# Kernel optimization log

Measured on AMD Instinct MI355X. Metric: run time of the kernel, lower is better.

## Reference

```python
import jax, jax.numpy as jnp
import numpy as np

N_USERS = 50000
N0, N1, N2 = 200000, 50000, 12500
E0, E1, E2 = 1600000, 400000, 100000
B = 128
NUMP, TWEET, CATP, DES = 6, 768, 2, 768
IN_DIM, HID = 128, 128
SLOPE = 0.01  # LeakyReLU default


def setup_inputs() -> dict:
    key = jax.random.key(0)
    ks = iter(jax.random.split(key, 32))
    f32 = jnp.float32
    nrm = lambda s, sc=0.05: jax.random.normal(next(ks), s, f32) * sc
    inp = {}
    inp['x_raw'] = jax.random.normal(next(ks), (N_USERS, NUMP + TWEET + CATP + DES), f32)
    inp['W_des'] = nrm((DES, IN_DIM // 4)); inp['b_des'] = jnp.zeros((IN_DIM // 4,), f32)
    inp['W_tweet'] = nrm((TWEET, IN_DIM // 4)); inp['b_tweet'] = jnp.zeros((IN_DIM // 4,), f32)
    inp['W_num'] = nrm((NUMP, IN_DIM // 4)); inp['b_num'] = jnp.zeros((IN_DIM // 4,), f32)
    inp['W_cat'] = nrm((CATP, IN_DIM // 4)); inp['b_cat'] = jnp.zeros((IN_DIM // 4,), f32)
    inp['W_in'] = nrm((IN_DIM, HID)); inp['b_in'] = jnp.zeros((HID,), f32)
    inp['prelu_a'] = jnp.full((HID,), 0.25, f32)
    inp['W_conv'] = nrm((3, HID, HID)); inp['b_conv'] = jnp.zeros((3, HID), f32)
    inp['Wc1'] = nrm((3 * HID, HID)); inp['bc1'] = jnp.zeros((HID,), f32)
    inp['Wc2'] = nrm((HID, HID)); inp['bc2'] = jnp.zeros((HID,), f32)
    ri = lambda n, hi: jax.random.randint(next(ks), (n,), 0, hi, jnp.int32)
    inp['nodelist'] = ri(N0, N_USERS)
    inp['e0'] = jnp.stack([ri(E0, N0), ri(E0, N0)])
    inp['e1'] = jnp.stack([ri(E1, N1), ri(E1, N1)])
    inp['e2'] = jnp.stack([ri(E2, N2), ri(E2, N2)])
    inp['parent1'] = ri(N0, N1)   # coarsening assignment layer0 -> layer1
    inp['parent2'] = ri(N1, N2)   # layer1 -> layer2
    inp['batch1'] = jnp.sort(ri(N1, B))
    inp['batch2'] = jnp.sort(ri(N2, B))
    return inp


def _leaky(x):
    return jnp.where(x > 0, x, SLOPE * x)


def _gcn(h, ei, W, b, n):
    # GCNConv: lin -> sym-normalized add-aggregation with self-loops -> +bias
    h = h @ W
    loop = jnp.arange(n, dtype=ei.dtype)
    src = jnp.concatenate([ei[0], loop])
    dst = jnp.concatenate([ei[1], loop])
    deg = jax.ops.segment_sum(jnp.ones(dst.shape, h.dtype), dst, num_segments=n)
    dinv = jnp.where(deg > 0, jax.lax.rsqrt(deg), 0.0)
    msg = h[src] * (dinv[src] * dinv[dst])[:, None]
    return jax.ops.segment_sum(msg, dst, num_segments=n) + b


def reference(x_raw, W_des, b_des, W_tweet, b_tweet, W_num, b_num, W_cat, b_cat,
              W_in, b_in, prelu_a, W_conv, b_conv, Wc1, bc1, Wc2, bc2,
              nodelist, e0, e1, e2, parent1, parent2, batch1, batch2):
    # FeatureEncoder (twibot-20 slicing order: num_prop | tweet | cat_prop | des)
    n = _leaky(x_raw[:, :NUMP] @ W_num + b_num)
    t = _leaky(x_raw[:, NUMP:NUMP + TWEET] @ W_tweet + b_tweet)
    c = _leaky(x_raw[:, NUMP + TWEET:NUMP + TWEET + CATP] @ W_cat + b_cat)
    d = _leaky(x_raw[:, NUMP + TWEET + CATP:] @ W_des + b_des)
    h = jnp.concatenate([d, t, n, c], axis=1) @ W_in + b_in
    enc = jnp.where(h > 0, h, prelu_a * h)  # PReLU

    x = enc[nodelist]  # [N0, HID] gather per batched nodelists
    edges = [e0, e1, e2]
    sizes = [N0, N1, N2]
    parents = [parent1, parent2]
    nxt = [N1, N2]
    xs = []
    for i in range(3):
        x = jax.nn.relu(_gcn(x, edges[i], W_conv[i], b_conv[i], sizes[i]))
        if i < 2:  # SEPooling: pure scatter-add onto parent nodes (nn unused in its forward)
            x = jax.nn.relu(jax.ops.segment_sum(x, parents[i], num_segments=nxt[i]))
        xs.append(x)
    pooled = jnp.concatenate([
        jax.ops.segment_sum(xs[0], batch1, num_segments=B),
        jax.ops.segment_sum(xs[1], batch2, num_segments=B),
        jax.ops.segment_sum(xs[2], batch2, num_segments=B),
    ], axis=1)  # global sum pool, batch at layer min(i+1, tree_depth-1)
    z = jax.nn.relu(pooled @ Wc1 + bc1)  # dropout inactive (eval)
    return z @ Wc2 + bc2
```

## Files before the change

kernel.cpp:

```cpp
#include <hip/hip_runtime.h>

#define N_USERS 50000
#define NN0 200000
#define NN1 50000
#define NN2 12500
#define EE0 1600000
#define EE1 400000
#define EE2 100000


__global__ __launch_bounds__(256) void k_enc3(
    const float* __restrict__ xr,
    const float* __restrict__ Wd, const float* __restrict__ bd,
    const float* __restrict__ Wt, const float* __restrict__ bt,
    const float* __restrict__ Wn, const float* __restrict__ bn,
    const float* __restrict__ Wc, const float* __restrict__ bc,
    float* __restrict__ h128)
{
    __shared__ float XsD[32][68];
    __shared__ float XsT[32][68];
    __shared__ float Ws[32][68];
    __shared__ float xnc[64][8];
    __shared__ float Wl[8][64];

    int t = threadIdx.x;
    int cg = t & 15, rg = t >> 4;
    int base = blockIdx.x * 64;

    if (t < 64) {
        int row = base + t;
        if (row < N_USERS) {
            const float* xp = xr + (size_t)row * 1544;
            float4 a = *(const float4*)xp;
            float2 b2 = *(const float2*)(xp + 4);
            float2 c2 = *(const float2*)(xp + 774);
            xnc[t][0] = a.x; xnc[t][1] = a.y; xnc[t][2] = a.z; xnc[t][3] = a.w;
            xnc[t][4] = b2.x; xnc[t][5] = b2.y; xnc[t][6] = c2.x; xnc[t][7] = c2.y;
        } else {
            #pragma unroll
            for (int k = 0; k < 8; k++) xnc[t][k] = 0.f;
        }
    } else if (t >= 192) {
        int l = t - 192;
        #pragma unroll
        for (int k = 0; k < 8; k++) {
            float w = 0.f;
            if (l < 32) { if (k < 6) w = Wn[k * 32 + l]; }
            else        { if (k >= 6) w = Wc[(k - 6) * 32 + (l - 32)]; }
            Wl[k][l] = w;
        }
    }

    float acc[4][4];
    #pragma unroll
    for (int r = 0; r < 4; r++)
        #pragma unroll
        for (int c = 0; c < 4; c++) acc[r][c] = 0.f;

    for (int kc = 0; kc < 768; kc += 32) {
        __syncthreads();
        #pragma unroll
        for (int h = 0; h < 2; h++) {
            int fi = t * 2 + h;
            int row = fi >> 3, q = fi & 7;
            int grow = base + row;
            float4 vd = {0.f, 0.f, 0.f, 0.f};
            float2 va = {0.f, 0.f}, vb = {0.f, 0.f};
            if (grow < N_USERS) {
                const float* xp = xr + (size_t)grow * 1544 + kc + q * 4;
                vd = *(const float4*)(xp + 776);
                va = *(const float2*)(xp + 6);
                vb = *(const float2*)(xp + 8);
            }
            int k0 = q * 4;
            XsD[k0 + 0][row] = vd.x; XsD[k0 + 1][row] = vd.y;
            XsD[k0 + 2][row] = vd.z; XsD[k0 + 3][row] = vd.w;
            XsT[k0 + 0][row] = va.x; XsT[k0 + 1][row] = va.y;
            XsT[k0 + 2][row] = vb.x; XsT[k0 + 3][row] = vb.y;
        }
        #pragma unroll
        for (int h = 0; h < 2; h++) {
            int fi = t + h * 256;
            int k = fi >> 4, c4 = (fi & 15) * 4;
            float4 w = (c4 < 32) ? *(const float4*)(Wd + (size_t)(kc + k) * 32 + c4)
                                 : *(const float4*)(Wt + (size_t)(kc + k) * 32 + (c4 - 32));
            *(float4*)&Ws[k][c4] = w;
        }
        __syncthreads();

        const float* Xp = (cg < 8) ? &XsD[0][0] : &XsT[0][0];
        #pragma unroll 8
        for (int k = 0; k < 32; k++) {
            float4 xv = *(const float4*)(Xp + k * 68 + rg * 4);
            float4 wv = *(const float4*)&Ws[k][cg * 4];
            acc[0][0] = fmaf(xv.x, wv.x, acc[0][0]);
            acc[0][1] = fmaf(xv.x, wv.y, acc[0][1]);
            acc[0][2] = fmaf(xv.x, wv.z, acc[0][2]);
            acc[0][3] = fmaf(xv.x, wv.w, acc[0][3]);
            acc[1][0] = fmaf(xv.y, wv.x, acc[1][0]);
            acc[1][1] = fmaf(xv.y, wv.y, acc[1][1]);
            acc[1][2] = fmaf(xv.y, wv.z, acc[1][2]);
            acc[1][3] = fmaf(xv.y, wv.w, acc[1][3]);
            acc[2][0] = fmaf(xv.z, wv.x, acc[2][0]);
            acc[2][1] = fmaf(xv.z, wv.y, acc[2][1]);
            acc[2][2] = fmaf(xv.z, wv.z, acc[2][2]);
            acc[2][3] = fmaf(xv.z, wv.w, acc[2][3]);
            acc[3][0] = fmaf(xv.w, wv.x, acc[3][0]);
            acc[3][1] = fmaf(xv.w, wv.y, acc[3][1]);
            acc[3][2] = fmaf(xv.w, wv.z, acc[3][2]);
            acc[3][3] = fmaf(xv.w, wv.w, acc[3][3]);
        }
    }

    float bh[4], bl[4], wlv[8][4];
    #pragma unroll
    for (int c = 0; c < 4; c++) {
        int j = cg * 4 + c;
        bh[c] = (j < 32) ? bd[j] : bt[j - 32];
        bl[c] = (j < 32) ? bn[j] : bc[j - 32];
        #pragma unroll
        for (int k = 0; k < 8; k++) wlv[k][c] = Wl[k][j];
    }
    #pragma unroll
    for (int r = 0; r < 4; r++) {
        int lr = rg * 4 + r;
        int row = base + lr;
        if (row >= N_USERS) break;
        float4 hv;
        float* ph = &hv.x;
        #pragma unroll
        for (int c = 0; c < 4; c++) {
            float v = acc[r][c] + bh[c];
            ph[c] = v > 0.f ? v : 0.01f * v;
        }
        *(float4*)(h128 + (size_t)row * 128 + cg * 4) = hv;
        float4 lv;
        float* pl = &lv.x;
        #pragma unroll
        for (int c = 0; c < 4; c++) {
            float v = bl[c];
            #pragma unroll
            for (int k = 0; k < 8; k++) v = fmaf(xnc[lr][k], wlv[k][c], v);
            pl[c] = v > 0.f ? v : 0.01f * v;
        }
        *(float4*)(h128 + (size_t)row * 128 + 64 + cg * 4) = lv;
    }
}

template<int EPI>
__global__ __launch_bounds__(256) void k_gemmT(
    const float* X, const float* __restrict__ W, const float* __restrict__ bias,
    const float* __restrict__ pa, float* OUT, int n)
{
    __shared__ float Xs[32][132];
    __shared__ float Ws[32][132];
    int t = threadIdx.x;
    int cg = t & 31, rg = t >> 5;
    int base = blockIdx.x * 32;

    #pragma unroll
    for (int h = 0; h < 4; h++) {
        int fi = t + h * 256;
        int row = fi >> 5, q = fi & 31;
        float4 v = {0.f, 0.f, 0.f, 0.f};
        if (base + row < n) v = *(const float4*)(X + (size_t)(base + row) * 128 + q * 4);
        *(float4*)&Xs[row][q * 4] = v;
    }

    float acc[4][4];
    #pragma unroll
    for (int r = 0; r < 4; r++)
        #pragma unroll
        for (int c = 0; c < 4; c++) acc[r][c] = 0.f;

    for (int kc = 0; kc < 128; kc += 32) {
        __syncthreads();
        #pragma unroll
        for (int h = 0; h < 4; h++) {
            int fi = t + h * 256;
            int k = fi >> 5, q = fi & 31;
            *(float4*)&Ws[k][q * 4] = *(const float4*)(W + (size_t)(kc + k) * 128 + q * 4);
        }
        __syncthreads();
        #pragma unroll
        for (int k4 = 0; k4 < 8; k4++) {
            int k = k4 * 4;
            float4 w0 = *(const float4*)&Ws[k + 0][cg * 4];
            float4 w1 = *(const float4*)&Ws[k + 1][cg * 4];
            float4 w2 = *(const float4*)&Ws[k + 2][cg * 4];
            float4 w3 = *(const float4*)&Ws[k + 3][cg * 4];
            #pragma unroll
            for (int r = 0; r < 4; r++) {
                float4 xv = *(const float4*)&Xs[rg * 4 + r][kc + k];
                acc[r][0] = fmaf(xv.w, w3.x, fmaf(xv.z, w2.x, fmaf(xv.y, w1.x, fmaf(xv.x, w0.x, acc[r][0]))));
                acc[r][1] = fmaf(xv.w, w3.y, fmaf(xv.z, w2.y, fmaf(xv.y, w1.y, fmaf(xv.x, w0.y, acc[r][1]))));
                acc[r][2] = fmaf(xv.w, w3.z, fmaf(xv.z, w2.z, fmaf(xv.y, w1.z, fmaf(xv.x, w0.z, acc[r][2]))));
                acc[r][3] = fmaf(xv.w, w3.w, fmaf(xv.z, w2.w, fmaf(xv.y, w1.w, fmaf(xv.x, w0.w, acc[r][3]))));
            }
        }
    }

    float4 bv = {0.f, 0.f, 0.f, 0.f}, pv = {0.f, 0.f, 0.f, 0.f};
    if (EPI == 1) { bv = *(const float4*)(bias + cg * 4); pv = *(const float4*)(pa + cg * 4); }
    #pragma unroll
    for (int r = 0; r < 4; r++) {
        int row = base + rg * 4 + r;
        if (row >= n) break;
        float4 v;
        if (EPI == 1) {
            v.x = acc[r][0] + bv.x; v.x = v.x > 0.f ? v.x : pv.x * v.x;
            v.y = acc[r][1] + bv.y; v.y = v.y > 0.f ? v.y : pv.y * v.y;
            v.z = acc[r][2] + bv.z; v.z = v.z > 0.f ? v.z : pv.z * v.z;
            v.w = acc[r][3] + bv.w; v.w = v.w > 0.f ? v.w : pv.w * v.w;
        } else {
            v.x = acc[r][0]; v.y = acc[r][1]; v.z = acc[r][2]; v.w = acc[r][3];
        }
        *(float4*)(OUT + (size_t)row * 128 + cg * 4) = v;
    }
}

__device__ __forceinline__ void seg_of_scanblk(int b, int& doff, int& bsoff, int& lb) {
    if (b < 196)      { doff = 0;      bsoff = 0;   lb = b; }
    else if (b < 245) { doff = 200704; bsoff = 196; lb = b - 196; }
    else if (b < 258) { doff = 250880; bsoff = 245; lb = b - 245; }
    else if (b < 307) { doff = 264192; bsoff = 258; lb = b - 258; }
    else              { doff = 314368; bsoff = 307; lb = b - 307; }
}

__global__ __launch_bounds__(256) void k_count_all(
    const int* __restrict__ d0, const int* __restrict__ d1, const int* __restrict__ d2,
    const int* __restrict__ p1, const int* __restrict__ p2,
    int* __restrict__ degs, int* __restrict__ ranks)
{
    int t0 = blockIdx.x * 256 + threadIdx.x;
    if (t0 >= 587500) return;
    #pragma unroll
    for (int k = 0; k < 4; k++) {
        int gid = t0 + k * 587500;
        int idx;
        if (gid < 1600000)      idx = d0[gid];
        else if (gid < 2000000) idx = 200704 + d1[gid - 1600000];
        else if (gid < 2100000) idx = 250880 + d2[gid - 2000000];
        else if (gid < 2300000) idx = 264192 + p1[gid - 2100000];
        else                    idx = 314368 + p2[gid - 2300000];
        ranks[gid] = atomicAdd(&degs[idx], 1);
    }
}

__global__ __launch_bounds__(256) void k_scan_all(
    const int* __restrict__ degs, int* __restrict__ rowsts, int* __restrict__ bsums)
{
    __shared__ int sh[256];
    int doff, bsoff, lb;
    seg_of_scanblk(blockIdx.x, doff, bsoff, lb);
    int t = threadIdx.x;
    int base = doff + lb * 1024 + t * 4;
    int v[4], s = 0;
    #pragma unroll
    for (int k = 0; k < 4; k++) { v[k] = degs[base + k]; s += v[k]; }
    sh[t] = s;
    __syncthreads();
    for (int off = 1; off < 256; off <<= 1) {
        int x = 0;
        if (t >= off) x = sh[t - off];
        __syncthreads();
        if (t >= off) sh[t] += x;
        __syncthreads();
    }
    int ex = sh[t] - s;
    if (t == 255) bsums[bsoff + lb] = sh[255];
    #pragma unroll
    for (int k = 0; k < 4; k++) { rowsts[base + k] = ex; ex += v[k]; }
}

__global__ __launch_bounds__(256) void k_scantop_all(int* __restrict__ bsums)
{
    __shared__ int sh[256];
    int b = blockIdx.x;
    int off0, nb;
    if (b == 0)      { off0 = 0;   nb = 196; }
    else if (b == 1) { off0 = 196; nb = 49; }
    else if (b == 2) { off0 = 245; nb = 13; }
    else if (b == 3) { off0 = 258; nb = 49; }
    else             { off0 = 307; nb = 13; }
    int t = threadIdx.x;
    int v = (t < nb) ? bsums[off0 + t] : 0;
    sh[t] = v;
    __syncthreads();
    for (int off = 1; off < 256; off <<= 1) {
        int x = 0;
        if (t >= off) x = sh[t - off];
        __syncthreads();
        if (t >= off) sh[t] += x;
        __syncthreads();
    }
    if (t < nb) bsums[off0 + t] = sh[t] - v;
}

__global__ __launch_bounds__(256) void k_scanadd_all(
    int* __restrict__ rowsts, const int* __restrict__ bsums,
    const int* __restrict__ degs, float* __restrict__ dinvs)
{
    int doff, bsoff, lb;
    seg_of_scanblk(blockIdx.x, doff, bsoff, lb);
    int t = threadIdx.x;
    int base = doff + lb * 1024 + t * 4;
    int add = bsums[bsoff + lb];
    bool dodinv = (doff <= 250880);
    #pragma unroll
    for (int k = 0; k < 4; k++) {
        int i = base + k;
        rowsts[i] += add;
        if (dodinv) dinvs[i] = rsqrtf((float)degs[i] + 1.0f);
    }
}

__global__ __launch_bounds__(256) void k_scatter_all(
    const int* __restrict__ s0, const int* __restrict__ d0,
    const int* __restrict__ s1, const int* __restrict__ d1,
    const int* __restrict__ s2, const int* __restrict__ d2,
    const int* __restrict__ p1, const int* __restrict__ p2,
    const int* __restrict__ rowsts, const int* __restrict__ ranks,
    int* __restrict__ elists)
{
    int t0 = blockIdx.x * 256 + threadIdx.x;
    if (t0 >= 587500) return;
    #pragma unroll
    for (int k = 0; k < 4; k++) {
        int gid = t0 + k * 587500;
        int idx, val, eloff;
        if (gid < 1600000)      { idx = d0[gid];                    val = s0[gid];           eloff = 0; }
        else if (gid < 2000000) { int i = gid - 1600000; idx = 200704 + d1[i]; val = s1[i]; eloff = 1600000; }
        else if (gid < 2100000) { int i = gid - 2000000; idx = 250880 + d2[i]; val = s2[i]; eloff = 2000000; }
        else if (gid < 2300000) { int i = gid - 2100000; idx = 264192 + p1[i]; val = i;     eloff = 2100000; }
        else                    { int i = gid - 2300000; idx = 314368 + p2[i]; val = i;     eloff = 2300000; }
        int p = rowsts[idx] + ranks[gid];
        elists[eloff + p] = val;
    }
}

__global__ __launch_bounds__(256) void k_gatherU(
    const float* __restrict__ U, const int* __restrict__ nl,
    const int* __restrict__ rowst, const int* __restrict__ elist,
    const float* __restrict__ dinv, const float* __restrict__ bias,
    float* __restrict__ out, int n)
{
    size_t gid = (size_t)blockIdx.x * 256 + threadIdx.x;
    int d = (int)(gid >> 5);
    if (d >= n) return;
    int l = (int)(gid & 31);
    const float4* Uv = (const float4*)U;
    float dd = dinv[d];
    float4 self = Uv[(size_t)nl[d] * 32 + l];
    float4 acc;
    acc.x = self.x * dd; acc.y = self.y * dd; acc.z = self.z * dd; acc.w = self.w * dd;
    int s0 = rowst[d], s1 = rowst[d + 1];
    for (int e = s0; e < s1; ++e) {
        int s = elist[e];
        float ds = dinv[s];
        float4 v = Uv[(size_t)nl[s] * 32 + l];
        acc.x = fmaf(v.x, ds, acc.x);
        acc.y = fmaf(v.y, ds, acc.y);
        acc.z = fmaf(v.z, ds, acc.z);
        acc.w = fmaf(v.w, ds, acc.w);
    }
    const float4 b = ((const float4*)bias)[l];
    float4 y;
    y.x = fmaxf(fmaf(acc.x, dd, b.x), 0.f);
    y.y = fmaxf(fmaf(acc.y, dd, b.y), 0.f);
    y.z = fmaxf(fmaf(acc.z, dd, b.z), 0.f);
    y.w = fmaxf(fmaf(acc.w, dd, b.w), 0.f);
    ((float4*)out)[(size_t)d * 32 + l] = y;
}

__global__ __launch_bounds__(256) void k_gather(
    const float* __restrict__ h, const int* __restrict__ rowst,
    const int* __restrict__ elist, const float* __restrict__ dinv,
    const float* __restrict__ bias, float* __restrict__ out, int n)
{
    size_t gid = (size_t)blockIdx.x * 256 + threadIdx.x;
    int d = (int)(gid >> 5);
    if (d >= n) return;
    int l = (int)(gid & 31);
    const float4* hv = (const float4*)h;
    float dd = dinv[d];
    float4 self = hv[(size_t)d * 32 + l];
    float4 acc;
    acc.x = self.x * dd; acc.y = self.y * dd; acc.z = self.z * dd; acc.w = self.w * dd;
    int s0 = rowst[d], s1 = rowst[d + 1];
    for (int e = s0; e < s1; ++e) {
        int s = elist[e];
        float ds = dinv[s];
        float4 v = hv[(size_t)s * 32 + l];
        acc.x = fmaf(v.x, ds, acc.x);
        acc.y = fmaf(v.y, ds, acc.y);
        acc.z = fmaf(v.z, ds, acc.z);
        acc.w = fmaf(v.w, ds, acc.w);
    }
    const float4 b = ((const float4*)bias)[l];
    float4 y;
    y.x = fmaxf(fmaf(acc.x, dd, b.x), 0.f);
    y.y = fmaxf(fmaf(acc.y, dd, b.y), 0.f);
    y.z = fmaxf(fmaf(acc.z, dd, b.z), 0.f);
    y.w = fmaxf(fmaf(acc.w, dd, b.w), 0.f);
    ((float4*)out)[(size_t)d * 32 + l] = y;
}

__global__ __launch_bounds__(256) void k_poolgather(
    const float* __restrict__ Y, const int* __restrict__ rowst,
    const int* __restrict__ elist, float* __restrict__ out, int np)
{
    size_t gid = (size_t)blockIdx.x * 256 + threadIdx.x;
    int p = (int)(gid >> 5);
    if (p >= np) return;
    int l = (int)(gid & 31);
    const float4* yv = (const float4*)Y;
    float4 acc = {0.f, 0.f, 0.f, 0.f};
    int s0 = rowst[p], s1 = rowst[p + 1];
    for (int e = s0; e < s1; ++e) {
        int i = elist[e];
        float4 v = yv[(size_t)i * 32 + l];
        acc.x += v.x; acc.y += v.y; acc.z += v.z; acc.w += v.w;
    }
    float4 y;
    y.x = fmaxf(acc.x, 0.f); y.y = fmaxf(acc.y, 0.f);
    y.z = fmaxf(acc.z, 0.f); y.w = fmaxf(acc.w, 0.f);
    ((float4*)out)[(size_t)p * 32 + l] = y;
}

__global__ __launch_bounds__(128) void k_bpool_all(
    const float* __restrict__ X1, const float* __restrict__ X2, const float* __restrict__ Y2,
    const int* __restrict__ b1, const int* __restrict__ b2, float* __restrict__ pl)
{
    int b = blockIdx.x;
    const float* src; const int* bidx; int coloff, n, r0;
    if (b < 391)      { src = X1; bidx = b1; coloff = 0;   n = 50000; r0 = b * 128; }
    else if (b < 489) { src = X2; bidx = b2; coloff = 128; n = 12500; r0 = (b - 391) * 128; }
    else              { src = Y2; bidx = b2; coloff = 256; n = 12500; r0 = (b - 489) * 128; }
    if (r0 >= n) return;
    int j = threadIdx.x;
    int r1 = min(r0 + 128, n);
    float acc = 0.f;
    int prev = bidx[r0];
    for (int r = r0; r < r1; ++r) {
        int bb = bidx[r];
        if (bb != prev) {
            unsafeAtomicAdd(&pl[(size_t)prev * 384 + coloff + j], acc);
            acc = 0.f; prev = bb;
        }
        acc += src[(size_t)r * 128 + j];
    }
    unsafeAtomicAdd(&pl[(size_t)prev * 384 + coloff + j], acc);
}

__global__ void k_mlp(const float* __restrict__ A, const float* __restrict__ W,
                      const float* __restrict__ b, float* __restrict__ out,
                      int K, int dorelu)
{
    __shared__ float as[384];
    int r = blockIdx.x, j = threadIdx.x;
    for (int i = j; i < K; i += 128) as[i] = A[(size_t)r * K + i];
    __syncthreads();
    float acc = b[j];
    for (int k = 0; k < K; k++) acc = fmaf(as[k], W[(size_t)k * 128 + j], acc);
    if (dorelu) acc = fmaxf(acc, 0.f);
    out[(size_t)r * 128 + j] = acc;
}

extern "C" void kernel_launch(void* const* d_in, const int* in_sizes, int n_in,
                              void* d_out, int out_size, void* d_ws, size_t ws_size,
                              hipStream_t stream)
{
    const float* x_raw  = (const float*)d_in[0];
    const float* W_des  = (const float*)d_in[1];
    const float* b_des  = (const float*)d_in[2];
    const float* W_twe  = (const float*)d_in[3];
    const float* b_twe  = (const float*)d_in[4];
    const float* W_num  = (const float*)d_in[5];
    const float* b_num  = (const float*)d_in[6];
    const float* W_cat  = (const float*)d_in[7];
    const float* b_cat  = (const float*)d_in[8];
    const float* W_in   = (const float*)d_in[9];
    const float* b_in   = (const float*)d_in[10];
    const float* prelua = (const float*)d_in[11];
    const float* W_conv = (const float*)d_in[12];
    const float* b_conv = (const float*)d_in[13];
    const float* Wc1    = (const float*)d_in[14];
    const float* bc1    = (const float*)d_in[15];
    const float* Wc2    = (const float*)d_in[16];
    const float* bc2    = (const float*)d_in[17];
    const int* nodelist = (const int*)d_in[18];
    const int* e0       = (const int*)d_in[19];
    const int* e1       = (const int*)d_in[20];
    const int* e2       = (const int*)d_in[21];
    const int* parent1  = (const int*)d_in[22];
    const int* parent2  = (const int*)d_in[23];
    const int* batch1   = (const int*)d_in[24];
    const int* batch2   = (const int*)d_in[25];

    float* WS  = (float*)d_ws;
    float* ENC = WS;
    int*   DEGS   = (int*)d_ws;
    int*   ROWSTS = DEGS + 327680;
    float* DINVS  = (float*)(ROWSTS + 327680);
    int*   BSUMS  = (int*)(DINVS + 264192);
    int*   RANKS  = BSUMS + 512;
    int*   ELISTS = RANKS + 2350000;
    float* U  = WS + 6400000;
    float* H  = WS + 12800000;
    float* Y  = WS + 19200000;
    float* X1 = WS + 44800000;
    float* X2 = WS + 51200000;
    float* PL = WS + 52800000;
    float* Z  = PL + 49152;

    hipMemsetAsync(PL, 0, (size_t)128 * 384 * 4, stream);

    k_enc3<<<(N_USERS + 63) / 64, 256, 0, stream>>>(
        x_raw, W_des, b_des, W_twe, b_twe, W_num, b_num, W_cat, b_cat, ENC);
    k_gemmT<1><<<(N_USERS + 31) / 32, 256, 0, stream>>>(
        ENC, W_in, b_in, prelua, ENC, N_USERS);
    k_gemmT<0><<<(N_USERS + 31) / 32, 256, 0, stream>>>(
        ENC, W_conv, nullptr, nullptr, U, N_USERS);

    hipMemsetAsync(DEGS, 0, (size_t)327680 * 4, stream);
    k_count_all<<<(587500 + 255) / 256, 256, 0, stream>>>(
        e0 + EE0, e1 + EE1, e2 + EE2, parent1, parent2, DEGS, RANKS);
    k_scan_all<<<320, 256, 0, stream>>>(DEGS, ROWSTS, BSUMS);
    k_scantop_all<<<5, 256, 0, stream>>>(BSUMS);
    k_scanadd_all<<<320, 256, 0, stream>>>(ROWSTS, BSUMS, DEGS, DINVS);
    k_scatter_all<<<(587500 + 255) / 256, 256, 0, stream>>>(
        e0, e0 + EE0, e1, e1 + EE1, e2, e2 + EE2, parent1, parent2,
        ROWSTS, RANKS, ELISTS);

    k_gatherU<<<(int)(((size_t)NN0 * 32 + 255) / 256), 256, 0, stream>>>(
        U, nodelist, ROWSTS, ELISTS, DINVS, b_conv, Y, NN0);
    k_poolgather<<<(int)(((size_t)NN1 * 32 + 255) / 256), 256, 0, stream>>>(
        Y, ROWSTS + 264192, ELISTS + 2100000, X1, NN1);

    k_gemmT<0><<<(NN1 + 31) / 32, 256, 0, stream>>>(
        X1, W_conv + 16384, nullptr, nullptr, H, NN1);
    k_gather<<<(int)(((size_t)NN1 * 32 + 255) / 256), 256, 0, stream>>>(
        H, ROWSTS + 200704, ELISTS + 1600000, DINVS + 200704, b_conv + 128, Y, NN1);
    k_poolgather<<<(int)(((size_t)NN2 * 32 + 255) / 256), 256, 0, stream>>>(
        Y, ROWSTS + 314368, ELISTS + 2300000, X2, NN2);

    k_gemmT<0><<<(NN2 + 31) / 32, 256, 0, stream>>>(
        X2, W_conv + 32768, nullptr, nullptr, H, NN2);
    k_gather<<<(int)(((size_t)NN2 * 32 + 255) / 256), 256, 0, stream>>>(
        H, ROWSTS + 250880, ELISTS + 2000000, DINVS + 250880, b_conv + 256, Y, NN2);

    k_bpool_all<<<587, 128, 0, stream>>>(X1, X2, Y, batch1, batch2, PL);

    k_mlp<<<128, 128, 0, stream>>>(PL, Wc1, bc1, Z, 384, 1);
    k_mlp<<<128, 128, 0, stream>>>(Z, Wc2, bc2, (float*)d_out, 128, 0);
}
```

Measured before the change: 753.5 us.

## Fuse GCN aggregation with pooling, chain encoder GEMMs, prefetch encoder tiles, merge MLP

Several fusions land together. The encoder's input-projection GEMM and the first conv-weight GEMM now run in one kernel that keeps the PReLU output in shared memory. Each GCN gather is fused with the following parent pooling, so per-node outputs Y are no longer written and re-read. The separate scan-top kernel is replaced by a per-block reduction inside scanadd, the two MLP launches are merged, and the k_enc3 loads are register-prefetched one K-chunk ahead. Together these cut launches and intermediate global traffic. The cost is more register pressure and work grouped by parent node, which may leave the load imbalanced across threads.

Result: slower. 848.6 us (+12.6%).

```diff
diff --git a/kernel.cpp b/kernel.cpp
--- a/kernel.cpp
+++ b/kernel.cpp
@@ -51,6 +51,31 @@
         }
     }
 
+    int srow[2], sq[2];
+    #pragma unroll
+    for (int h = 0; h < 2; h++) { int fi = t * 2 + h; srow[h] = fi >> 3; sq[h] = fi & 7; }
+    bool vr[2];
+    #pragma unroll
+    for (int h = 0; h < 2; h++) vr[h] = (base + srow[h]) < N_USERS;
+
+    float4 pvd[2]; float2 pva[2], pvb[2]; float4 pw[2];
+
+    #pragma unroll
+    for (int h = 0; h < 2; h++) {
+        pvd[h] = make_float4(0.f, 0.f, 0.f, 0.f);
+        pva[h] = make_float2(0.f, 0.f); pvb[h] = make_float2(0.f, 0.f);
+        if (vr[h]) {
+            const float* xp = xr + (size_t)(base + srow[h]) * 1544 + sq[h] * 4;
+            pvd[h] = *(const float4*)(xp + 776);
+            pva[h] = *(const float2*)(xp + 6);
+            pvb[h] = *(const float2*)(xp + 8);
+        }
+        int fi = t + h * 256;
+        int k = fi >> 4, c4 = (fi & 15) * 4;
+        pw[h] = (c4 < 32) ? *(const float4*)(Wd + (size_t)k * 32 + c4)
+                          : *(const float4*)(Wt + (size_t)k * 32 + (c4 - 32));
+    }
+
     float acc[4][4];
     #pragma unroll
     for (int r = 0; r < 4; r++)
@@ -61,32 +86,32 @@
         __syncthreads();
         #pragma unroll
         for (int h = 0; h < 2; h++) {
-            int fi = t * 2 + h;
-            int row = fi >> 3, q = fi & 7;
-            int grow = base + row;
-            float4 vd = {0.f, 0.f, 0.f, 0.f};
-            float2 va = {0.f, 0.f}, vb = {0.f, 0.f};
-            if (grow < N_USERS) {
-                const float* xp = xr + (size_t)grow * 1544 + kc + q * 4;
-                vd = *(const float4*)(xp + 776);
-                va = *(const float2*)(xp + 6);
-                vb = *(const float2*)(xp + 8);
-            }
-            int k0 = q * 4;
-            XsD[k0 + 0][row] = vd.x; XsD[k0 + 1][row] = vd.y;
-            XsD[k0 + 2][row] = vd.z; XsD[k0 + 3][row] = vd.w;
-            XsT[k0 + 0][row] = va.x; XsT[k0 + 1][row] = va.y;
-            XsT[k0 + 2][row] = vb.x; XsT[k0 + 3][row] = vb.y;
-        }
-        #pragma unroll
-        for (int h = 0; h < 2; h++) {
+            int k0 = sq[h] * 4, row = srow[h];
+            XsD[k0 + 0][row] = pvd[h].x; XsD[k0 + 1][row] = pvd[h].y;
+            XsD[k0 + 2][row] = pvd[h].z; XsD[k0 + 3][row] = pvd[h].w;
+            XsT[k0 + 0][row] = pva[h].x; XsT[k0 + 1][row] = pva[h].y;
+            XsT[k0 + 2][row] = pvb[h].x; XsT[k0 + 3][row] = pvb[h].y;
             int fi = t + h * 256;
             int k = fi >> 4, c4 = (fi & 15) * 4;
-            float4 w = (c4 < 32) ? *(const float4*)(Wd + (size_t)(kc + k) * 32 + c4)
-                                 : *(const float4*)(Wt + (size_t)(kc + k) * 32 + (c4 - 32));
-            *(float4*)&Ws[k][c4] = w;
-        }
-        __syncthreads();
+            *(float4*)&Ws[k][c4] = pw[h];
+        }
+        __syncthreads();
+        int kn = kc + 32;
+        if (kn < 768) {
+            #pragma unroll
+            for (int h = 0; h < 2; h++) {
+                if (vr[h]) {
+                    const float* xp = xr + (size_t)(base + srow[h]) * 1544 + kn + sq[h] * 4;
+                    pvd[h] = *(const float4*)(xp + 776);
+                    pva[h] = *(const float2*)(xp + 6);
+                    pvb[h] = *(const float2*)(xp + 8);
+                }
+                int fi = t + h * 256;
+                int k = fi >> 4, c4 = (fi & 15) * 4;
+                pw[h] = (c4 < 32) ? *(const float4*)(Wd + (size_t)(kn + k) * 32 + c4)
+                                  : *(const float4*)(Wt + (size_t)(kn + k) * 32 + (c4 - 32));
+            }
+        }
 
         const float* Xp = (cg < 8) ? &XsD[0][0] : &XsT[0][0];
         #pragma unroll 8
@@ -147,10 +172,10 @@
     }
 }
 
-template<int EPI>
-__global__ __launch_bounds__(256) void k_gemmT(
-    const float* X, const float* __restrict__ W, const float* __restrict__ bias,
-    const float* __restrict__ pa, float* OUT, int n)
+__global__ __launch_bounds__(256) void k_gemm2(
+    const float* __restrict__ X, const float* __restrict__ W1,
+    const float* __restrict__ b1, const float* __restrict__ pa,
+    const float* __restrict__ W2, float* __restrict__ OUT, int n)
 {
     __shared__ float Xs[32][132];
     __shared__ float Ws[32][132];
@@ -179,7 +204,7 @@
         for (int h = 0; h < 4; h++) {
             int fi = t + h * 256;
             int k = fi >> 5, q = fi & 31;
-            *(float4*)&Ws[k][q * 4] = *(const float4*)(W + (size_t)(kc + k) * 128 + q * 4);
+            *(float4*)&Ws[k][q * 4] = *(const float4*)(W1 + (size_t)(kc + k) * 128 + q * 4);
         }
         __syncthreads();
         #pragma unroll
@@ -200,21 +225,116 @@
         }
     }
 
-    float4 bv = {0.f, 0.f, 0.f, 0.f}, pv = {0.f, 0.f, 0.f, 0.f};
-    if (EPI == 1) { bv = *(const float4*)(bias + cg * 4); pv = *(const float4*)(pa + cg * 4); }
+    float4 bv = *(const float4*)(b1 + cg * 4);
+    float4 pv = *(const float4*)(pa + cg * 4);
+    __syncthreads();
+    #pragma unroll
+    for (int r = 0; r < 4; r++) {
+        float v0 = acc[r][0] + bv.x; v0 = v0 > 0.f ? v0 : pv.x * v0;
+        float v1 = acc[r][1] + bv.y; v1 = v1 > 0.f ? v1 : pv.y * v1;
+        float v2 = acc[r][2] + bv.z; v2 = v2 > 0.f ? v2 : pv.z * v2;
+        float v3 = acc[r][3] + bv.w; v3 = v3 > 0.f ? v3 : pv.w * v3;
+        Xs[rg * 4 + r][cg * 4 + 0] = v0;
+        Xs[rg * 4 + r][cg * 4 + 1] = v1;
+        Xs[rg * 4 + r][cg * 4 + 2] = v2;
+        Xs[rg * 4 + r][cg * 4 + 3] = v3;
+        acc[r][0] = 0.f; acc[r][1] = 0.f; acc[r][2] = 0.f; acc[r][3] = 0.f;
+    }
+
+    for (int kc = 0; kc < 128; kc += 32) {
+        __syncthreads();
+        #pragma unroll
+        for (int h = 0; h < 4; h++) {
+            int fi = t + h * 256;
+            int k = fi >> 5, q = fi & 31;
+            *(float4*)&Ws[k][q * 4] = *(const float4*)(W2 + (size_t)(kc + k) * 128 + q * 4);
+        }
+        __syncthreads();
+        #pragma unroll
+        for (int k4 = 0; k4 < 8; k4++) {
+            int k = k4 * 4;
+            float4 w0 = *(const float4*)&Ws[k + 0][cg * 4];
+            float4 w1 = *(const float4*)&Ws[k + 1][cg * 4];
+            float4 w2 = *(const float4*)&Ws[k + 2][cg * 4];
+            float4 w3 = *(const float4*)&Ws[k + 3][cg * 4];
+            #pragma unroll
+            for (int r = 0; r < 4; r++) {
+                float4 xv = *(const float4*)&Xs[rg * 4 + r][kc + k];
+                acc[r][0] = fmaf(xv.w, w3.x, fmaf(xv.z, w2.x, fmaf(xv.y, w1.x, fmaf(xv.x, w0.x, acc[r][0]))));
+                acc[r][1] = fmaf(xv.w, w3.y, fmaf(xv.z, w2.y, fmaf(xv.y, w1.y, fmaf(xv.x, w0.y, acc[r][1]))));
+                acc[r][2] = fmaf(xv.w, w3.z, fmaf(xv.z, w2.z, fmaf(xv.y, w1.z, fmaf(xv.x, w0.z, acc[r][2]))));
+                acc[r][3] = fmaf(xv.w, w3.w, fmaf(xv.z, w2.w, fmaf(xv.y, w1.w, fmaf(xv.x, w0.w, acc[r][3]))));
+            }
+        }
+    }
+
     #pragma unroll
     for (int r = 0; r < 4; r++) {
         int row = base + rg * 4 + r;
         if (row >= n) break;
         float4 v;
-        if (EPI == 1) {
-            v.x = acc[r][0] + bv.x; v.x = v.x > 0.f ? v.x : pv.x * v.x;
-            v.y = acc[r][1] + bv.y; v.y = v.y > 0.f ? v.y : pv.y * v.y;
-            v.z = acc[r][2] + bv.z; v.z = v.z > 0.f ? v.z : pv.z * v.z;
-            v.w = acc[r][3] + bv.w; v.w = v.w > 0.f ? v.w : pv.w * v.w;
-        } else {
-            v.x = acc[r][0]; v.y = acc[r][1]; v.z = acc[r][2]; v.w = acc[r][3];
-        }
+        v.x = acc[r][0]; v.y = acc[r][1]; v.z = acc[r][2]; v.w = acc[r][3];
+        *(float4*)(OUT + (size_t)row * 128 + cg * 4) = v;
+    }
+}
+
+__global__ __launch_bounds__(256) void k_gemmT(
+    const float* X, const float* __restrict__ W, float* OUT, int n)
+{
+    __shared__ float Xs[32][132];
+    __shared__ float Ws[32][132];
+    int t = threadIdx.x;
+    int cg = t & 31, rg = t >> 5;
+    int base = blockIdx.x * 32;
+
+    #pragma unroll
+    for (int h = 0; h < 4; h++) {
+        int fi = t + h * 256;
+        int row = fi >> 5, q = fi & 31;
+        float4 v = {0.f, 0.f, 0.f, 0.f};
+        if (base + row < n) v = *(const float4*)(X + (size_t)(base + row) * 128 + q * 4);
+        *(float4*)&Xs[row][q * 4] = v;
+    }
+
+    float acc[4][4];
+    #pragma unroll
+    for (int r = 0; r < 4; r++)
+        #pragma unroll
+        for (int c = 0; c < 4; c++) acc[r][c] = 0.f;
+
+    for (int kc = 0; kc < 128; kc += 32) {
+        __syncthreads();
+        #pragma unroll
+        for (int h = 0; h < 4; h++) {
+            int fi = t + h * 256;
+            int k = fi >> 5, q = fi & 31;
+            *(float4*)&Ws[k][q * 4] = *(const float4*)(W + (size_t)(kc + k) * 128 + q * 4);
+        }
+        __syncthreads();
+        #pragma unroll
+        for (int k4 = 0; k4 < 8; k4++) {
+            int k = k4 * 4;
+            float4 w0 = *(const float4*)&Ws[k + 0][cg * 4];
+            float4 w1 = *(const float4*)&Ws[k + 1][cg * 4];
+            float4 w2 = *(const float4*)&Ws[k + 2][cg * 4];
+            float4 w3 = *(const float4*)&Ws[k + 3][cg * 4];
+            #pragma unroll
+            for (int r = 0; r < 4; r++) {
+                float4 xv = *(const float4*)&Xs[rg * 4 + r][kc + k];
+                acc[r][0] = fmaf(xv.w, w3.x, fmaf(xv.z, w2.x, fmaf(xv.y, w1.x, fmaf(xv.x, w0.x, acc[r][0]))));
+                acc[r][1] = fmaf(xv.w, w3.y, fmaf(xv.z, w2.y, fmaf(xv.y, w1.y, fmaf(xv.x, w0.y, acc[r][1]))));
+                acc[r][2] = fmaf(xv.w, w3.z, fmaf(xv.z, w2.z, fmaf(xv.y, w1.z, fmaf(xv.x, w0.z, acc[r][2]))));
+                acc[r][3] = fmaf(xv.w, w3.w, fmaf(xv.z, w2.w, fmaf(xv.y, w1.w, fmaf(xv.x, w0.w, acc[r][3]))));
+            }
+        }
+    }
+
+    #pragma unroll
+    for (int r = 0; r < 4; r++) {
+        int row = base + rg * 4 + r;
+        if (row >= n) break;
+        float4 v;
+        v.x = acc[r][0]; v.y = acc[r][1]; v.z = acc[r][2]; v.w = acc[r][3];
         *(float4*)(OUT + (size_t)row * 128 + cg * 4) = v;
     }
 }
@@ -273,39 +393,23 @@
     for (int k = 0; k < 4; k++) { rowsts[base + k] = ex; ex += v[k]; }
 }
 
-__global__ __launch_bounds__(256) void k_scantop_all(int* __restrict__ bsums)
-{
-    __shared__ int sh[256];
-    int b = blockIdx.x;
-    int off0, nb;
-    if (b == 0)      { off0 = 0;   nb = 196; }
-    else if (b == 1) { off0 = 196; nb = 49; }
-    else if (b == 2) { off0 = 245; nb = 13; }
-    else if (b == 3) { off0 = 258; nb = 49; }
-    else             { off0 = 307; nb = 13; }
-    int t = threadIdx.x;
-    int v = (t < nb) ? bsums[off0 + t] : 0;
-    sh[t] = v;
-    __syncthreads();
-    for (int off = 1; off < 256; off <<= 1) {
-        int x = 0;
-        if (t >= off) x = sh[t - off];
-        __syncthreads();
-        if (t >= off) sh[t] += x;
-        __syncthreads();
-    }
-    if (t < nb) bsums[off0 + t] = sh[t] - v;
-}
-
 __global__ __launch_bounds__(256) void k_scanadd_all(
     int* __restrict__ rowsts, const int* __restrict__ bsums,
     const int* __restrict__ degs, float* __restrict__ dinvs)
 {
+    __shared__ int sh[256];
     int doff, bsoff, lb;
     seg_of_scanblk(blockIdx.x, doff, bsoff, lb);
     int t = threadIdx.x;
+    sh[t] = (t < lb) ? bsums[bsoff + t] : 0;
+    __syncthreads();
+    #pragma unroll
+    for (int off = 128; off >= 1; off >>= 1) {
+        if (t < off) sh[t] += sh[t + off];
+        __syncthreads();
+    }
+    int add = sh[0];
     int base = doff + lb * 1024 + t * 4;
-    int add = bsums[bsoff + lb];
     bool dodinv = (doff <= 250880);
     #pragma unroll
     for (int k = 0; k < 4; k++) {
@@ -339,38 +443,84 @@
     }
 }
 
-__global__ __launch_bounds__(256) void k_gatherU(
+__global__ __launch_bounds__(256) void k_gcnpoolU(
     const float* __restrict__ U, const int* __restrict__ nl,
-    const int* __restrict__ rowst, const int* __restrict__ elist,
+    const int* __restrict__ rowstE, const int* __restrict__ elistE,
     const float* __restrict__ dinv, const float* __restrict__ bias,
-    float* __restrict__ out, int n)
+    const int* __restrict__ prowst, const int* __restrict__ pelist,
+    float* __restrict__ out, int np)
 {
     size_t gid = (size_t)blockIdx.x * 256 + threadIdx.x;
-    int d = (int)(gid >> 5);
-    if (d >= n) return;
+    int p = (int)(gid >> 5);
+    if (p >= np) return;
     int l = (int)(gid & 31);
     const float4* Uv = (const float4*)U;
-    float dd = dinv[d];
-    float4 self = Uv[(size_t)nl[d] * 32 + l];
-    float4 acc;
-    acc.x = self.x * dd; acc.y = self.y * dd; acc.z = self.z * dd; acc.w = self.w * dd;
-    int s0 = rowst[d], s1 = rowst[d + 1];
-    for (int e = s0; e < s1; ++e) {
-        int s = elist[e];
-        float ds = dinv[s];
-        float4 v = Uv[(size_t)nl[s] * 32 + l];
-        acc.x = fmaf(v.x, ds, acc.x);
-        acc.y = fmaf(v.y, ds, acc.y);
-        acc.z = fmaf(v.z, ds, acc.z);
-        acc.w = fmaf(v.w, ds, acc.w);
-    }
     const float4 b = ((const float4*)bias)[l];
+    float4 acc = {0.f, 0.f, 0.f, 0.f};
+    int c0 = prowst[p], c1 = prowst[p + 1];
+    for (int c = c0; c < c1; ++c) {
+        int d = pelist[c];
+        float dd = dinv[d];
+        float4 self = Uv[(size_t)nl[d] * 32 + l];
+        float4 a;
+        a.x = self.x * dd; a.y = self.y * dd; a.z = self.z * dd; a.w = self.w * dd;
+        int e0 = rowstE[d], e1 = rowstE[d + 1];
+        for (int e = e0; e < e1; ++e) {
+            int s = elistE[e];
+            float ds = dinv[s];
+            float4 v = Uv[(size_t)nl[s] * 32 + l];
+            a.x = fmaf(v.x, ds, a.x); a.y = fmaf(v.y, ds, a.y);
+            a.z = fmaf(v.z, ds, a.z); a.w = fmaf(v.w, ds, a.w);
+        }
+        acc.x += fmaxf(fmaf(a.x, dd, b.x), 0.f);
+        acc.y += fmaxf(fmaf(a.y, dd, b.y), 0.f);
+        acc.z += fmaxf(fmaf(a.z, dd, b.z), 0.f);
+        acc.w += fmaxf(fmaf(a.w, dd, b.w), 0.f);
+    }
     float4 y;
-    y.x = fmaxf(fmaf(acc.x, dd, b.x), 0.f);
-    y.y = fmaxf(fmaf(acc.y, dd, b.y), 0.f);
-    y.z = fmaxf(fmaf(acc.z, dd, b.z), 0.f);
-    y.w = fmaxf(fmaf(acc.w, dd, b.w), 0.f);
-    ((float4*)out)[(size_t)d * 32 + l] = y;
+    y.x = fmaxf(acc.x, 0.f); y.y = fmaxf(acc.y, 0.f);
+    y.z = fmaxf(acc.z, 0.f); y.w = fmaxf(acc.w, 0.f);
+    ((float4*)out)[(size_t)p * 32 + l] = y;
+}
+
+__global__ __launch_bounds__(256) void k_gcnpool(
+    const float* __restrict__ h,
+    const int* __restrict__ rowstE, const int* __restrict__ elistE,
+    const float* __restrict__ dinv, const float* __restrict__ bias,
+    const int* __restrict__ prowst, const int* __restrict__ pelist,
+    float* __restrict__ out, int np)
+{
+    size_t gid = (size_t)blockIdx.x * 256 + threadIdx.x;
+    int p = (int)(gid >> 5);
+    if (p >= np) return;
+    int l = (int)(gid & 31);
+    const float4* hv = (const float4*)h;
+    const float4 b = ((const float4*)bias)[l];
+    float4 acc = {0.f, 0.f, 0.f, 0.f};
+    int c0 = prowst[p], c1 = prowst[p + 1];
+    for (int c = c0; c < c1; ++c) {
+        int d = pelist[c];
+        float dd = dinv[d];
+        float4 self = hv[(size_t)d * 32 + l];
+        float4 a;
+        a.x = self.x * dd; a.y = self.y * dd; a.z = self.z * dd; a.w = self.w * dd;
+        int e0 = rowstE[d], e1 = rowstE[d + 1];
+        for (int e = e0; e < e1; ++e) {
+            int s = elistE[e];
+            float ds = dinv[s];
+            float4 v = hv[(size_t)s * 32 + l];
+            a.x = fmaf(v.x, ds, a.x); a.y = fmaf(v.y, ds, a.y);
+            a.z = fmaf(v.z, ds, a.z); a.w = fmaf(v.w, ds, a.w);
+        }
+        acc.x += fmaxf(fmaf(a.x, dd, b.x), 0.f);
+        acc.y += fmaxf(fmaf(a.y, dd, b.y), 0.f);
+        acc.z += fmaxf(fmaf(a.z, dd, b.z), 0.f);
+        acc.w += fmaxf(fmaf(a.w, dd, b.w), 0.f);
+    }
+    float4 y;
+    y.x = fmaxf(acc.x, 0.f); y.y = fmaxf(acc.y, 0.f);
+    y.z = fmaxf(acc.z, 0.f); y.w = fmaxf(acc.w, 0.f);
+    ((float4*)out)[(size_t)p * 32 + l] = y;
 }
 
 __global__ __launch_bounds__(256) void k_gather(
@@ -406,28 +556,6 @@
     ((float4*)out)[(size_t)d * 32 + l] = y;
 }
 
-__global__ __launch_bounds__(256) void k_poolgather(
-    const float* __restrict__ Y, const int* __restrict__ rowst,
-    const int* __restrict__ elist, float* __restrict__ out, int np)
-{
-    size_t gid = (size_t)blockIdx.x * 256 + threadIdx.x;
-    int p = (int)(gid >> 5);
-    if (p >= np) return;
-    int l = (int)(gid & 31);
-    const float4* yv = (const float4*)Y;
-    float4 acc = {0.f, 0.f, 0.f, 0.f};
-    int s0 = rowst[p], s1 = rowst[p + 1];
-    for (int e = s0; e < s1; ++e) {
-        int i = elist[e];
-        float4 v = yv[(size_t)i * 32 + l];
-        acc.x += v.x; acc.y += v.y; acc.z += v.z; acc.w += v.w;
-    }
-    float4 y;
-    y.x = fmaxf(acc.x, 0.f); y.y = fmaxf(acc.y, 0.f);
-    y.z = fmaxf(acc.z, 0.f); y.w = fmaxf(acc.w, 0.f);
-    ((float4*)out)[(size_t)p * 32 + l] = y;
-}
-
 __global__ __launch_bounds__(128) void k_bpool_all(
     const float* __restrict__ X1, const float* __restrict__ X2, const float* __restrict__ Y2,
     const int* __restrict__ b1, const int* __restrict__ b2, float* __restrict__ pl)
@@ -453,18 +581,25 @@
     unsafeAtomicAdd(&pl[(size_t)prev * 384 + coloff + j], acc);
 }
 
-__global__ void k_mlp(const float* __restrict__ A, const float* __restrict__ W,
-                      const float* __restrict__ b, float* __restrict__ out,
-                      int K, int dorelu)
+__global__ void k_mlp2(const float* __restrict__ PL,
+                       const float* __restrict__ Wc1, const float* __restrict__ bc1,
+                       const float* __restrict__ Wc2, const float* __restrict__ bc2,
+                       float* __restrict__ out)
 {
     __shared__ float as[384];
+    __shared__ float zs[128];
     int r = blockIdx.x, j = threadIdx.x;
-    for (int i = j; i < K; i += 128) as[i] = A[(size_t)r * K + i];
+    as[j] = PL[(size_t)r * 384 + j];
+    as[j + 128] = PL[(size_t)r * 384 + 128 + j];
+    as[j + 256] = PL[(size_t)r * 384 + 256 + j];
     __syncthreads();
-    float acc = b[j];
-    for (int k = 0; k < K; k++) acc = fmaf(as[k], W[(size_t)k * 128 + j], acc);
-    if (dorelu) acc = fmaxf(acc, 0.f);
-    out[(size_t)r * 128 + j] = acc;
+    float acc = bc1[j];
+    for (int k = 0; k < 384; k++) acc = fmaf(as[k], Wc1[(size_t)k * 128 + j], acc);
+    zs[j] = fmaxf(acc, 0.f);
+    __syncthreads();
+    float o = bc2[j];
+    for (int k = 0; k < 128; k++) o = fmaf(zs[k], Wc2[(size_t)k * 128 + j], o);
+    out[(size_t)r * 128 + j] = o;
 }
 
 extern "C" void kernel_launch(void* const* d_in, const int* in_sizes, int n_in,
@@ -512,46 +647,37 @@
     float* X1 = WS + 44800000;
     float* X2 = WS + 51200000;
     float* PL = WS + 52800000;
-    float* Z  = PL + 49152;
 
     hipMemsetAsync(PL, 0, (size_t)128 * 384 * 4, stream);
 
     k_enc3<<<(N_USERS + 63) / 64, 256, 0, stream>>>(
         x_raw, W_des, b_des, W_twe, b_twe, W_num, b_num, W_cat, b_cat, ENC);
-    k_gemmT<1><<<(N_USERS + 31) / 32, 256, 0, stream>>>(
-        ENC, W_in, b_in, prelua, ENC, N_USERS);
-    k_gemmT<0><<<(N_USERS + 31) / 32, 256, 0, stream>>>(
-        ENC, W_conv, nullptr, nullptr, U, N_USERS);
+    k_gemm2<<<(N_USERS + 31) / 32, 256, 0, stream>>>(
+        ENC, W_in, b_in, prelua, W_conv, U, N_USERS);
 
     hipMemsetAsync(DEGS, 0, (size_t)327680 * 4, stream);
     k_count_all<<<(587500 + 255) / 256, 256, 0, stream>>>(
         e0 + EE0, e1 + EE1, e2 + EE2, parent1, parent2, DEGS, RANKS);
     k_scan_all<<<320, 256, 0, stream>>>(DEGS, ROWSTS, BSUMS);
-    k_scantop_all<<<5, 256, 0, stream>>>(BSUMS);
     k_scanadd_all<<<320, 256, 0, stream>>>(ROWSTS, BSUMS, DEGS, DINVS);
     k_scatter_all<<<(587500 + 255) / 256, 256, 0, stream>>>(
         e0, e0 + EE0, e1, e1 + EE1, e2, e2 + EE2, parent1, parent2,
         ROWSTS, RANKS, ELISTS);
 
-    k_gatherU<<<(int)(((size_t)NN0 * 32 + 255) / 256), 256, 0, stream>>>(
-        U, nodelist, ROWSTS, ELISTS, DINVS, b_conv, Y, NN0);
-    k_poolgather<<<(int)(((size_t)NN1 * 32 + 255) / 256), 256, 0, stream>>>(
-        Y, ROWSTS + 264192, ELISTS + 2100000, X1, NN1);
-
-    k_gemmT<0><<<(NN1 + 31) / 32, 256, 0, stream>>>(
-        X1, W_conv + 16384, nullptr, nullptr, H, NN1);
-    k_gather<<<(int)(((size_t)NN1 * 32 + 255) / 256), 256, 0, stream>>>(
-        H, ROWSTS + 200704, ELISTS + 1600000, DINVS + 200704, b_conv + 128, Y, NN1);
-    k_poolgather<<<(int)(((size_t)NN2 * 32 + 255) / 256), 256, 0, stream>>>(
-        Y, ROWSTS + 314368, ELISTS + 2300000, X2, NN2);
-
-    k_gemmT<0><<<(NN2 + 31) / 32, 256, 0, stream>>>(
-        X2, W_conv + 32768, nullptr, nullptr, H, NN2);
+    k_gcnpoolU<<<(int)(((size_t)NN1 * 32 + 255) / 256), 256, 0, stream>>>(
+        U, nodelist, ROWSTS, ELISTS, DINVS, b_conv,
+        ROWSTS + 264192, ELISTS + 2100000, X1, NN1);
+
+    k_gemmT<<<(NN1 + 31) / 32, 256, 0, stream>>>(X1, W_conv + 16384, H, NN1);
+    k_gcnpool<<<(int)(((size_t)NN2 * 32 + 255) / 256), 256, 0, stream>>>(
+        H, ROWSTS + 200704, ELISTS + 1600000, DINVS + 200704, b_conv + 128,
+        ROWSTS + 314368, ELISTS + 2300000, X2, NN2);
+
+    k_gemmT<<<(NN2 + 31) / 32, 256, 0, stream>>>(X2, W_conv + 32768, H, NN2);
     k_gather<<<(int)(((size_t)NN2 * 32 + 255) / 256), 256, 0, stream>>>(
         H, ROWSTS + 250880, ELISTS + 2000000, DINVS + 250880, b_conv + 256, Y, NN2);
 
     k_bpool_all<<<587, 128, 0, stream>>>(X1, X2, Y, batch1, batch2, PL);
 
-    k_mlp<<<128, 128, 0, stream>>>(PL, Wc1, bc1, Z, 384, 1);
-    k_mlp<<<128, 128, 0, stream>>>(Z, Wc2, bc2, (float*)d_out, 128, 0);
-}
+    k_mlp2<<<128, 128, 0, stream>>>(PL, Wc1, bc1, Wc2, bc2, (float*)d_out);
+}
```
